# Kernel tuning notes

Hardware: AMD Instinct MI355X
Metric: run time of the kernel (lower is better)

Reference implementation:

```python
import jax, jax.numpy as jnp
import numpy as np


def setup_inputs() -> dict:
    key = jax.random.key(0)
    k1, k2, k3 = jax.random.split(key, 3)
    B, N, D, A = 64, 500000, 512, 7
    batch_rep = jax.random.normal(k1, (B, D), dtype=jnp.float32)
    representations = jax.random.normal(k2, (N, D), dtype=jnp.float32)
    actions = jax.random.normal(k3, (N, A), dtype=jnp.float32)
    return {
        "batch_rep": batch_rep,
        "representations": representations,
        "actions": actions,
        "k": 16,
    }


def reference(batch_rep, representations, actions, k):
    # torch.cdist (p=2): pairwise Euclidean distances [B, N] via the
    d2 = (
        jnp.sum(batch_rep * batch_rep, axis=1, keepdims=True)
        - 2.0 * (batch_rep @ representations.T)
        + jnp.sum(representations * representations, axis=1)[None, :]
    )
    dist = jnp.sqrt(jnp.maximum(d2, 0.0))  # [B, N]

    # torch.topk(largest=False): smallest-k distances == top-k of negated.
    neg_top, indices = jax.lax.top_k(-dist, k)  # [B, k]
    top_k_dist = -neg_top

    # weights = softmax(-dist) over the k neighbors
    weights = jax.nn.softmax(-top_k_dist, axis=1)  # [B, k]

    top_k_actions = actions[indices]  # gather -> [B, k, A]
    pred = jnp.sum(top_k_actions * weights[..., None], axis=1)  # [B, A]
    return pred, indices
```

## Files before the change

### kernel.cpp

```cpp
#include <hip/hip_runtime.h>
#include <stdint.h>

typedef _Float16 f16;
typedef _Float16 f16x8 __attribute__((ext_vector_type(8)));
typedef float f32x4 __attribute__((ext_vector_type(4)));

#define INF_F __builtin_inff()
#define INF_I 0x7fffffff
#define KM 24
#define SCALE 262144.0f

__device__ __forceinline__ bool lexLess(float s1, int n1, float s2, int n2) {
    return (s1 < s2) || (s1 == s2 && n1 < n2);
}
__device__ __forceinline__ bool lexLessI(int s1, int n1, int s2, int n2) {
    return (s1 < s2) || (s1 == s2 && n1 < n2);
}

__device__ __forceinline__ uint4 pack8(const float4 a, const float4 b) {
    const auto p0 = __builtin_amdgcn_cvt_pkrtz(a.x, a.y);
    const auto p1 = __builtin_amdgcn_cvt_pkrtz(a.z, a.w);
    const auto p2 = __builtin_amdgcn_cvt_pkrtz(b.x, b.y);
    const auto p3 = __builtin_amdgcn_cvt_pkrtz(b.z, b.w);
    uint4 u;
    u.x = __builtin_bit_cast(unsigned, p0);
    u.y = __builtin_bit_cast(unsigned, p1);
    u.z = __builtin_bit_cast(unsigned, p2);
    u.w = __builtin_bit_cast(unsigned, p3);
    return u;
}

__global__ __launch_bounds__(512, 4) void dist_topk_kernel(
    const float* __restrict__ reps, const float* __restrict__ brep,
    float* __restrict__ cs, int* __restrict__ ci,
    int N, int TT, int NBLK)
{
    __shared__ int slds[64][65];
    __shared__ int topdI[16][64];
    __shared__ int topiI[16][64];
    __shared__ int thrS[64], thrnS[64], cntS[64];

    const int tid = threadIdx.x;
    const int w = tid >> 6, lane = tid & 63;
    const int li = lane & 15, q = lane >> 4;
    const int b = blockIdx.x;
    const int kbase = 64 * w + 8 * q;

    uint4 a[2][4];
    #pragma unroll
    for (int ks2 = 0; ks2 < 2; ks2++)
        #pragma unroll
        for (int mt = 0; mt < 4; mt++) {
            const float* src = brep + (mt * 16 + li) * 512 + kbase + 32 * ks2;
            const float4 x0 = *(const float4*)(src);
            const float4 x1 = *(const float4*)(src + 4);
            a[ks2][mt] = pack8(x0, x1);
        }

    if (tid < 64) { thrS[tid] = INF_I; thrnS[tid] = INF_I; cntS[tid] = 0; }
    for (int i = tid; i < 64 * 65; i += 512) ((int*)slds)[i] = 0;
    __syncthreads();

    float4 yA0, yA1;
    {
        const int r0 = min(b * 64 + li, N - 1);
        const float* p = reps + (size_t)r0 * 512 + kbase;
        yA0 = *(const float4*)(p);
        yA1 = *(const float4*)(p + 4);
    }

    int sc = 0;
    for (int t = b; t < TT; t += NBLK, sc++) {
        const int n0 = t * 64;

        f32x4 acc0, acc1, acc2, acc3;
        float yn = 0.f;

        #pragma unroll
        for (int s = 0; s < 8; s++) {
            const int nsub = s >> 1, ks2 = s & 1;
            float4 yB0, yB1;
            {
                int nt0, ns;
                if (s < 7) { nt0 = n0; ns = s + 1; }
                else       { nt0 = min(t + NBLK, TT - 1) * 64; ns = 0; }
                const int rr = min(nt0 + (ns >> 1) * 16 + li, N - 1);
                const float* p = reps + (size_t)rr * 512 + kbase + 32 * (ns & 1);
                yB0 = *(const float4*)(p);
                yB1 = *(const float4*)(p + 4);
            }
            if (ks2 == 0) {
                acc0 = (f32x4){0.f,0.f,0.f,0.f}; acc1 = (f32x4){0.f,0.f,0.f,0.f};
                acc2 = (f32x4){0.f,0.f,0.f,0.f}; acc3 = (f32x4){0.f,0.f,0.f,0.f};
                yn = 0.f;
            }
            yn = fmaf(yA0.x, yA0.x, fmaf(yA0.y, yA0.y, fmaf(yA0.z, yA0.z, fmaf(yA0.w, yA0.w, yn))));
            yn = fmaf(yA1.x, yA1.x, fmaf(yA1.y, yA1.y, fmaf(yA1.z, yA1.z, fmaf(yA1.w, yA1.w, yn))));
            const f16x8 bf = __builtin_bit_cast(f16x8, pack8(yA0, yA1));
            acc0 = __builtin_amdgcn_mfma_f32_16x16x32_f16(__builtin_bit_cast(f16x8, a[ks2][0]), bf, acc0, 0, 0, 0);
            acc1 = __builtin_amdgcn_mfma_f32_16x16x32_f16(__builtin_bit_cast(f16x8, a[ks2][1]), bf, acc1, 0, 0, 0);
            acc2 = __builtin_amdgcn_mfma_f32_16x16x32_f16(__builtin_bit_cast(f16x8, a[ks2][2]), bf, acc2, 0, 0, 0);
            acc3 = __builtin_amdgcn_mfma_f32_16x16x32_f16(__builtin_bit_cast(f16x8, a[ks2][3]), bf, acc3, 0, 0, 0);
            if (ks2 == 1) {
                float ys = yn;
                ys += __shfl_xor(ys, 16);
                ys += __shfl_xor(ys, 32);
                const int nloc = nsub * 16 + li;
                if (q == 0) atomicAdd(&slds[nloc][64], __float2int_rn(ys * SCALE));
                #pragma unroll
                for (int jj = 0; jj < 4; jj++) {
                    atomicAdd(&slds[nloc][ 0 + 4 * q + jj], __float2int_rn(acc0[jj] * SCALE));
                    atomicAdd(&slds[nloc][16 + 4 * q + jj], __float2int_rn(acc1[jj] * SCALE));
                    atomicAdd(&slds[nloc][32 + 4 * q + jj], __float2int_rn(acc2[jj] * SCALE));
                    atomicAdd(&slds[nloc][48 + 4 * q + jj], __float2int_rn(acc3[jj] * SCALE));
                }
            }
            yA0 = yB0; yA1 = yB1;
        }

        __syncthreads();

        if (w == (sc & 7)) {
            const int r = lane;
            const int* sb = &slds[0][0];
            int thr = thrS[r], thrn = thrnS[r], cnt = cntS[r];
            for (int j = 0; j < 64; j++) {
                const int n = n0 + j;
                if (n >= N) break;
                const int s = sb[j * 65 + 64] - 2 * sb[j * 65 + r];
                if (lexLessI(s, n, thr, thrn)) {
                    if (cnt < 16) {
                        topdI[cnt][r] = s; topiI[cnt][r] = n; cnt++;
                        if (cnt == 16) {
                            int tv = topdI[0][r], tn = topiI[0][r];
                            #pragma unroll
                            for (int u = 1; u < 16; u++) {
                                int v = topdI[u][r], nn = topiI[u][r];
                                if (!lexLessI(v, nn, tv, tn)) { tv = v; tn = nn; }
                            }
                            thr = tv; thrn = tn;
                        }
                    } else {
                        #pragma unroll
                        for (int u = 0; u < 16; u++)
                            if (topdI[u][r] == thr && topiI[u][r] == thrn) {
                                topdI[u][r] = s; topiI[u][r] = n; break;
                            }
                        int tv = topdI[0][r], tn = topiI[0][r];
                        #pragma unroll
                        for (int u = 1; u < 16; u++) {
                            int v = topdI[u][r], nn = topiI[u][r];
                            if (!lexLessI(v, nn, tv, tn)) { tv = v; tn = nn; }
                        }
                        thr = tv; thrn = tn;
                    }
                }
            }
            thrS[r] = thr; thrnS[r] = thrn; cntS[r] = cnt;
            for (int e2 = lane; e2 < 64 * 65; e2 += 64) (&slds[0][0])[e2] = 0;
        }

        __syncthreads();
    }

    __syncthreads();
    if (tid < 64) {
        const int c = cntS[tid];
        const size_t base = ((size_t)b * 64 + tid) * 16;
        for (int j = 0; j < 16; j++) {
            cs[base + j] = (j < c) ? ((float)topdI[j][tid] * (1.0f / SCALE)) : INF_F;
            ci[base + j] = (j < c) ? topiI[j][tid] : INF_I;
        }
    }
}

__global__ __launch_bounds__(256) void merge_kernel(
    const float* __restrict__ cs, const int* __restrict__ ci,
    const float* __restrict__ brep, const float* __restrict__ reps,
    const float* __restrict__ acts,
    float* __restrict__ out, int NLISTS, int N, int BA)
{
    const int r = blockIdx.x;
    const int tid = threadIdx.x;
    __shared__ __align__(16) float xrow[512];
    __shared__ float S1s[256 * KM];
    __shared__ int   S1i[256 * KM];
    __shared__ float S2s[32 * KM];
    __shared__ int   S2i[32 * KM];
    __shared__ double fd[KM];
    __shared__ int    fn[KM];

    if (tid < 128)
        *(float4*)(&xrow[tid * 4]) = *(const float4*)(&brep[(size_t)r * 512 + tid * 4]);

    float ls[KM]; int li[KM];
    #pragma unroll
    for (int j = 0; j < KM; j++) { ls[j] = INF_F; li[j] = INF_I; }
    float mv = INF_F; int mn = INF_I; int mp = 0;
    const int total = NLISTS * 16;
    for (int e = tid; e < total; e += 256) {
        const int blk = e >> 4, j = e & 15;
        const size_t a = (size_t)blk * 1024 + (size_t)r * 16 + j;
        const float s = cs[a]; const int n = ci[a];
        if (lexLess(s, n, mv, mn)) {
            ls[mp] = s; li[mp] = n;
            mv = ls[0]; mn = li[0]; mp = 0;
            #pragma unroll
            for (int u = 1; u < KM; u++)
                if (!lexLess(ls[u], li[u], mv, mn)) { mv = ls[u]; mn = li[u]; mp = u; }
        }
    }
    #pragma unroll
    for (int j = 0; j < KM; j++) { S1s[tid * KM + j] = ls[j]; S1i[tid * KM + j] = li[j]; }
    __syncthreads();

    if (tid < 32) {
        #pragma unroll
        for (int j = 0; j < KM; j++) { ls[j] = INF_F; li[j] = INF_I; }
        mv = INF_F; mn = INF_I; mp = 0;
        for (int e = tid * 8 * KM; e < (tid * 8 + 8) * KM; e++) {
            const float s = S1s[e]; const int n = S1i[e];
            if (lexLess(s, n, mv, mn)) {
                ls[mp] = s; li[mp] = n;
                mv = ls[0]; mn = li[0]; mp = 0;
                #pragma unroll
                for (int u = 1; u < KM; u++)
                    if (!lexLess(ls[u], li[u], mv, mn)) { mv = ls[u]; mn = li[u]; mp = u; }
            }
        }
        #pragma unroll
        for (int j = 0; j < KM; j++) { S2s[tid * KM + j] = ls[j]; S2i[tid * KM + j] = li[j]; }
    }
    __syncthreads();

    if (tid == 0) {
        #pragma unroll
        for (int j = 0; j < KM; j++) { ls[j] = INF_F; li[j] = INF_I; }
        mv = INF_F; mn = INF_I; mp = 0;
        for (int e = 0; e < 32 * KM; e++) {
            const float s = S2s[e]; const int n = S2i[e];
            if (lexLess(s, n, mv, mn)) {
                ls[mp] = s; li[mp] = n;
                mv = ls[0]; mn = li[0]; mp = 0;
                #pragma unroll
                for (int u = 1; u < KM; u++)
                    if (!lexLess(ls[u], li[u], mv, mn)) { mv = ls[u]; mn = li[u]; mp = u; }
            }
        }
        for (int j = 0; j < KM; j++) fn[j] = li[j];
    }
    __syncthreads();

    if (tid < KM) {
        const int n = fn[tid];
        double d = 1.0e300;
        if (n >= 0 && n < N) {
            d = 0.0;
            const float* yp = reps + (size_t)n * 512;
            for (int i = 0; i < 512; i += 4) {
                float4 yv = *(const float4*)(yp + i);
                double d0 = (double)xrow[i + 0] - (double)yv.x;
                double d1 = (double)xrow[i + 1] - (double)yv.y;
                double d2 = (double)xrow[i + 2] - (double)yv.z;
                double d3 = (double)xrow[i + 3] - (double)yv.w;
                d += d0 * d0 + d1 * d1 + d2 * d2 + d3 * d3;
            }
        }
        fd[tid] = d;
    }
    __syncthreads();

    if (tid == 0) {
        int ord[KM];
        for (int j = 0; j < KM; j++) ord[j] = j;
        for (int a = 0; a < 16; a++) {
            int best = a;
            for (int u = a + 1; u < KM; u++) {
                const int ou = ord[u], ob = ord[best];
                if (fd[ou] < fd[ob] || (fd[ou] == fd[ob] && fn[ou] < fn[ob])) best = u;
            }
            int tmp = ord[a]; ord[a] = ord[best]; ord[best] = tmp;
        }
        double dist[16];
        for (int j = 0; j < 16; j++) {
            double v = fd[ord[j]];
            dist[j] = sqrt(v > 0.0 ? v : 0.0);
        }
        double wv[16], wsum = 0.0;
        for (int j = 0; j < 16; j++) { wv[j] = exp(dist[0] - dist[j]); wsum += wv[j]; }
        for (int a = 0; a < 7; a++) {
            double s = 0.0;
            for (int j = 0; j < 16; j++)
                s += wv[j] * (double)acts[(size_t)fn[ord[j]] * 7 + a];
            out[r * 7 + a] = (float)(s / wsum);
        }
        for (int j = 0; j < 16; j++)
            out[BA + r * 16 + j] = (float)fn[ord[j]];
    }
}

extern "C" void kernel_launch(void* const* d_in, const int* in_sizes, int n_in,
                              void* d_out, int out_size, void* d_ws, size_t ws_size,
                              hipStream_t stream) {
    const float* brep = (const float*)d_in[0];
    const float* reps = (const float*)d_in[1];
    const float* acts = (const float*)d_in[2];
    const int D = 512;
    const int B = in_sizes[0] / D;
    const int N = in_sizes[1] / D;
    float* out = (float*)d_out;

    int NBLK = 512;
    const size_t perblk = (size_t)64 * 16 * 8;
    while (NBLK > 1 && (size_t)NBLK * perblk > ws_size) NBLK >>= 1;

    float* cs = (float*)d_ws;
    int* ci = (int*)((char*)d_ws + (size_t)NBLK * 64 * 16 * 4);

    const int TT = (N + 63) / 64;

    dist_topk_kernel<<<NBLK, 512, 0, stream>>>(reps, brep, cs, ci, N, TT, NBLK);
    merge_kernel<<<B, 256, 0, stream>>>(cs, ci, brep, reps, acts, out, NBLK, N, B * 7);
}
```

Measured before the change: 1.470 ms.

## Stage representation tiles through LDS with double buffering and overlapped top-k scan

The distance kernel now processes 16-row tiles. Each tile is loaded with coalesced row-contiguous global reads, converted to fp16 into a double-buffered LDS tile, and its squared norms are reduced by a wave shuffle. The per-query top-k scan for the previous tile runs in the same iteration as the MFMA work for the current one, so each iteration needs one barrier instead of two full-block syncs. This aims to hide global load latency and cut barrier stalls, at the cost of more LDS use and smaller tiles, which means more iterations. The merge kernel also splits its double-precision distance sum into four independent accumulators to break the dependency chain.

Result: slower. 1.600 ms (+8.8%).

```diff
diff --git a/kernel.cpp b/kernel.cpp
--- a/kernel.cpp
+++ b/kernel.cpp
@@ -29,13 +29,28 @@
     u.w = __builtin_bit_cast(unsigned, p3);
     return u;
 }
+__device__ __forceinline__ uint2 pack4(const float4 a) {
+    const auto p0 = __builtin_amdgcn_cvt_pkrtz(a.x, a.y);
+    const auto p1 = __builtin_amdgcn_cvt_pkrtz(a.z, a.w);
+    uint2 u;
+    u.x = __builtin_bit_cast(unsigned, p0);
+    u.y = __builtin_bit_cast(unsigned, p1);
+    return u;
+}
+__device__ __forceinline__ float ssum(const float4 v) {
+    return fmaf(v.x, v.x, fmaf(v.y, v.y, fmaf(v.z, v.z, v.w * v.w)));
+}
+
+#define YROWB 1040
 
 __global__ __launch_bounds__(512, 4) void dist_topk_kernel(
     const float* __restrict__ reps, const float* __restrict__ brep,
     float* __restrict__ cs, int* __restrict__ ci,
     int N, int TT, int NBLK)
 {
-    __shared__ int slds[64][65];
+    __shared__ __align__(16) char ybuf[2][16 * YROWB];
+    __shared__ int slds[2][16][65];
+    __shared__ int ynI[3][16];
     __shared__ int topdI[16][64];
     __shared__ int topiI[16][64];
     __shared__ int thrS[64], thrnS[64], cntS[64];
@@ -44,108 +59,65 @@
     const int w = tid >> 6, lane = tid & 63;
     const int li = lane & 15, q = lane >> 4;
     const int b = blockIdx.x;
-    const int kbase = 64 * w + 8 * q;
 
     uint4 a[2][4];
     #pragma unroll
     for (int ks2 = 0; ks2 < 2; ks2++)
         #pragma unroll
         for (int mt = 0; mt < 4; mt++) {
-            const float* src = brep + (mt * 16 + li) * 512 + kbase + 32 * ks2;
-            const float4 x0 = *(const float4*)(src);
-            const float4 x1 = *(const float4*)(src + 4);
-            a[ks2][mt] = pack8(x0, x1);
+            const float* src = brep + (mt * 16 + li) * 512 + 64 * w + 32 * ks2 + 8 * q;
+            a[ks2][mt] = pack8(*(const float4*)(src), *(const float4*)(src + 4));
         }
 
     if (tid < 64) { thrS[tid] = INF_I; thrnS[tid] = INF_I; cntS[tid] = 0; }
-    for (int i = tid; i < 64 * 65; i += 512) ((int*)slds)[i] = 0;
-    __syncthreads();
-
-    float4 yA0, yA1;
-    {
-        const int r0 = min(b * 64 + li, N - 1);
-        const float* p = reps + (size_t)r0 * 512 + kbase;
-        yA0 = *(const float4*)(p);
-        yA1 = *(const float4*)(p + 4);
-    }
-
-    int sc = 0;
-    for (int t = b; t < TT; t += NBLK, sc++) {
-        const int n0 = t * 64;
-
-        f32x4 acc0, acc1, acc2, acc3;
-        float yn = 0.f;
-
-        #pragma unroll
-        for (int s = 0; s < 8; s++) {
-            const int nsub = s >> 1, ks2 = s & 1;
-            float4 yB0, yB1;
-            {
-                int nt0, ns;
-                if (s < 7) { nt0 = n0; ns = s + 1; }
-                else       { nt0 = min(t + NBLK, TT - 1) * 64; ns = 0; }
-                const int rr = min(nt0 + (ns >> 1) * 16 + li, N - 1);
-                const float* p = reps + (size_t)rr * 512 + kbase + 32 * (ns & 1);
-                yB0 = *(const float4*)(p);
-                yB1 = *(const float4*)(p + 4);
-            }
-            if (ks2 == 0) {
-                acc0 = (f32x4){0.f,0.f,0.f,0.f}; acc1 = (f32x4){0.f,0.f,0.f,0.f};
-                acc2 = (f32x4){0.f,0.f,0.f,0.f}; acc3 = (f32x4){0.f,0.f,0.f,0.f};
-                yn = 0.f;
-            }
-            yn = fmaf(yA0.x, yA0.x, fmaf(yA0.y, yA0.y, fmaf(yA0.z, yA0.z, fmaf(yA0.w, yA0.w, yn))));
-            yn = fmaf(yA1.x, yA1.x, fmaf(yA1.y, yA1.y, fmaf(yA1.z, yA1.z, fmaf(yA1.w, yA1.w, yn))));
-            const f16x8 bf = __builtin_bit_cast(f16x8, pack8(yA0, yA1));
-            acc0 = __builtin_amdgcn_mfma_f32_16x16x32_f16(__builtin_bit_cast(f16x8, a[ks2][0]), bf, acc0, 0, 0, 0);
-            acc1 = __builtin_amdgcn_mfma_f32_16x16x32_f16(__builtin_bit_cast(f16x8, a[ks2][1]), bf, acc1, 0, 0, 0);
-            acc2 = __builtin_amdgcn_mfma_f32_16x16x32_f16(__builtin_bit_cast(f16x8, a[ks2][2]), bf, acc2, 0, 0, 0);
-            acc3 = __builtin_amdgcn_mfma_f32_16x16x32_f16(__builtin_bit_cast(f16x8, a[ks2][3]), bf, acc3, 0, 0, 0);
-            if (ks2 == 1) {
-                float ys = yn;
-                ys += __shfl_xor(ys, 16);
-                ys += __shfl_xor(ys, 32);
-                const int nloc = nsub * 16 + li;
-                if (q == 0) atomicAdd(&slds[nloc][64], __float2int_rn(ys * SCALE));
-                #pragma unroll
-                for (int jj = 0; jj < 4; jj++) {
-                    atomicAdd(&slds[nloc][ 0 + 4 * q + jj], __float2int_rn(acc0[jj] * SCALE));
-                    atomicAdd(&slds[nloc][16 + 4 * q + jj], __float2int_rn(acc1[jj] * SCALE));
-                    atomicAdd(&slds[nloc][32 + 4 * q + jj], __float2int_rn(acc2[jj] * SCALE));
-                    atomicAdd(&slds[nloc][48 + 4 * q + jj], __float2int_rn(acc3[jj] * SCALE));
-                }
-            }
-            yA0 = yB0; yA1 = yB1;
-        }
-
-        __syncthreads();
-
-        if (w == (sc & 7)) {
-            const int r = lane;
-            const int* sb = &slds[0][0];
-            int thr = thrS[r], thrn = thrnS[r], cnt = cntS[r];
-            for (int j = 0; j < 64; j++) {
-                const int n = n0 + j;
-                if (n >= N) break;
-                const int s = sb[j * 65 + 64] - 2 * sb[j * 65 + r];
-                if (lexLessI(s, n, thr, thrn)) {
-                    if (cnt < 16) {
-                        topdI[cnt][r] = s; topiI[cnt][r] = n; cnt++;
-                        if (cnt == 16) {
-                            int tv = topdI[0][r], tn = topiI[0][r];
-                            #pragma unroll
-                            for (int u = 1; u < 16; u++) {
-                                int v = topdI[u][r], nn = topiI[u][r];
-                                if (!lexLessI(v, nn, tv, tn)) { tv = v; tn = nn; }
-                            }
-                            thr = tv; thrn = tn;
-                        }
-                    } else {
-                        #pragma unroll
-                        for (int u = 0; u < 16; u++)
-                            if (topdI[u][r] == thr && topiI[u][r] == thrn) {
-                                topdI[u][r] = s; topiI[u][r] = n; break;
-                            }
+    for (int i = tid; i < 2 * 16 * 65; i += 512) ((int*)slds)[i] = 0;
+
+    const int myCnt = (TT - b + NBLK - 1) / NBLK;
+
+    float4 st[4];
+    auto issue = [&](int t) {
+        const int r0 = t * 16 + 2 * w;
+        #pragma unroll
+        for (int i = 0; i < 4; i++) {
+            int rr = r0 + (i >> 1); if (rr >= N) rr = N - 1;
+            st[i] = *(const float4*)((const char*)(reps + (size_t)rr * 512)
+                                     + (i & 1) * 1024 + lane * 16);
+        }
+    };
+    auto cvt_write = [&](int yb, int yi) {
+        char* base = ybuf[yb];
+        #pragma unroll
+        for (int i = 0; i < 4; i++) {
+            const uint2 u = pack4(st[i]);
+            *(uint2*)(base + (2 * w + (i >> 1)) * YROWB
+                      + ((i & 1) * 256 + lane * 4) * 2) = u;
+        }
+        float s0 = ssum(st[0]) + ssum(st[1]);
+        float s1 = ssum(st[2]) + ssum(st[3]);
+        #pragma unroll
+        for (int d = 1; d < 64; d <<= 1) {
+            s0 += __shfl_xor(s0, d);
+            s1 += __shfl_xor(s1, d);
+        }
+        if (lane == 0) {
+            ynI[yi][2 * w]     = __float2int_rn(s0 * SCALE);
+            ynI[yi][2 * w + 1] = __float2int_rn(s1 * SCALE);
+        }
+    };
+    auto scan = [&](int sp) {
+        const int n0p = (b + sp * NBLK) * 16;
+        const int r = lane;
+        volatile int* sb = &slds[sp & 1][0][0];
+        volatile int* yb = &ynI[sp % 3][0];
+        int thr = thrS[r], thrn = thrnS[r], cnt = cntS[r];
+        for (int j = 0; j < 16; j++) {
+            const int n = n0p + j;
+            if (n >= N) break;
+            const int s = yb[j] - 2 * sb[j * 65 + r];
+            if (lexLessI(s, n, thr, thrn)) {
+                if (cnt < 16) {
+                    topdI[cnt][r] = s; topiI[cnt][r] = n; cnt++;
+                    if (cnt == 16) {
                         int tv = topdI[0][r], tn = topiI[0][r];
                         #pragma unroll
                         for (int u = 1; u < 16; u++) {
@@ -154,16 +126,67 @@
                         }
                         thr = tv; thrn = tn;
                     }
+                } else {
+                    #pragma unroll
+                    for (int u = 0; u < 16; u++)
+                        if (topdI[u][r] == thr && topiI[u][r] == thrn) {
+                            topdI[u][r] = s; topiI[u][r] = n; break;
+                        }
+                    int tv = topdI[0][r], tn = topiI[0][r];
+                    #pragma unroll
+                    for (int u = 1; u < 16; u++) {
+                        int v = topdI[u][r], nn = topiI[u][r];
+                        if (!lexLessI(v, nn, tv, tn)) { tv = v; tn = nn; }
+                    }
+                    thr = tv; thrn = tn;
                 }
             }
-            thrS[r] = thr; thrnS[r] = thrn; cntS[r] = cnt;
-            for (int e2 = lane; e2 < 64 * 65; e2 += 64) (&slds[0][0])[e2] = 0;
-        }
-
-        __syncthreads();
-    }
-
-    __syncthreads();
+        }
+        thrS[r] = thr; thrnS[r] = thrn; cntS[r] = cnt;
+        for (int e2 = lane; e2 < 16 * 65; e2 += 64) sb[e2] = 0;
+    };
+
+    issue(b);
+    cvt_write(0, 0);
+    __syncthreads();
+
+    int sc = 0;
+    for (int t = b; t < TT; t += NBLK, ++sc) {
+        const int tb = sc & 1;
+        const bool haveNext = (t + NBLK) < TT;
+
+        if (haveNext) issue(t + NBLK);
+        __builtin_amdgcn_sched_barrier(0);
+
+        f32x4 acc0 = {0.f,0.f,0.f,0.f}, acc1 = {0.f,0.f,0.f,0.f};
+        f32x4 acc2 = {0.f,0.f,0.f,0.f}, acc3 = {0.f,0.f,0.f,0.f};
+        #pragma unroll
+        for (int ks2 = 0; ks2 < 2; ks2++) {
+            const f16x8 bf = *(const f16x8*)(ybuf[tb] + li * YROWB
+                                             + 128 * w + 64 * ks2 + 16 * q);
+            acc0 = __builtin_amdgcn_mfma_f32_16x16x32_f16(__builtin_bit_cast(f16x8, a[ks2][0]), bf, acc0, 0, 0, 0);
+            acc1 = __builtin_amdgcn_mfma_f32_16x16x32_f16(__builtin_bit_cast(f16x8, a[ks2][1]), bf, acc1, 0, 0, 0);
+            acc2 = __builtin_amdgcn_mfma_f32_16x16x32_f16(__builtin_bit_cast(f16x8, a[ks2][2]), bf, acc2, 0, 0, 0);
+            acc3 = __builtin_amdgcn_mfma_f32_16x16x32_f16(__builtin_bit_cast(f16x8, a[ks2][3]), bf, acc3, 0, 0, 0);
+        }
+        #pragma unroll
+        for (int jj = 0; jj < 4; jj++) {
+            atomicAdd(&slds[tb][li][ 0 + 4 * q + jj], __float2int_rn(acc0[jj] * SCALE));
+            atomicAdd(&slds[tb][li][16 + 4 * q + jj], __float2int_rn(acc1[jj] * SCALE));
+            atomicAdd(&slds[tb][li][32 + 4 * q + jj], __float2int_rn(acc2[jj] * SCALE));
+            atomicAdd(&slds[tb][li][48 + 4 * q + jj], __float2int_rn(acc3[jj] * SCALE));
+        }
+        if (sc > 0 && w == ((sc - 1) & 7)) scan(sc - 1);
+        if (haveNext) cvt_write(tb ^ 1, (sc + 1) % 3);
+        asm volatile("s_waitcnt lgkmcnt(0)");
+        __builtin_amdgcn_sched_barrier(0);
+        __builtin_amdgcn_s_barrier();
+        __builtin_amdgcn_sched_barrier(0);
+    }
+
+    if (w == ((myCnt - 1) & 7)) scan(myCnt - 1);
+    __syncthreads();
+
     if (tid < 64) {
         const int c = cntS[tid];
         const size_t base = ((size_t)b * 64 + tid) * 16;
@@ -255,16 +278,17 @@
         const int n = fn[tid];
         double d = 1.0e300;
         if (n >= 0 && n < N) {
-            d = 0.0;
+            double d0a = 0.0, d1a = 0.0, d2a = 0.0, d3a = 0.0;
             const float* yp = reps + (size_t)n * 512;
             for (int i = 0; i < 512; i += 4) {
                 float4 yv = *(const float4*)(yp + i);
-                double d0 = (double)xrow[i + 0] - (double)yv.x;
-                double d1 = (double)xrow[i + 1] - (double)yv.y;
-                double d2 = (double)xrow[i + 2] - (double)yv.z;
-                double d3 = (double)xrow[i + 3] - (double)yv.w;
-                d += d0 * d0 + d1 * d1 + d2 * d2 + d3 * d3;
-            }
+                double e0 = (double)xrow[i + 0] - (double)yv.x;
+                double e1 = (double)xrow[i + 1] - (double)yv.y;
+                double e2 = (double)xrow[i + 2] - (double)yv.z;
+                double e3 = (double)xrow[i + 3] - (double)yv.w;
+                d0a += e0 * e0; d1a += e1 * e1; d2a += e2 * e2; d3a += e3 * e3;
+            }
+            d = (d0a + d1a) + (d2a + d3a);
         }
         fd[tid] = d;
     }
@@ -317,7 +341,7 @@
     float* cs = (float*)d_ws;
     int* ci = (int*)((char*)d_ws + (size_t)NBLK * 64 * 16 * 4);
 
-    const int TT = (N + 63) / 64;
+    const int TT = (N + 15) / 16;
 
     dist_topk_kernel<<<NBLK, 512, 0, stream>>>(reps, brep, cs, ci, N, TT, NBLK);
     merge_kernel<<<B, 256, 0, stream>>>(cs, ci, brep, reps, acts, out, NBLK, N, B * 7);
```
